# Optimization experiments

Measured on AMD Instinct MI355X. Metric: run time of the kernel, lower is better.

Reference implementation:

```python
import jax, jax.numpy as jnp
import numpy as np

# ---- hyperparameters (from init_kwargs) ----
SIGMA, RHO = 1.0, 10.0
ALPHA, BETA = 1.0, 1.0
K = 3  # ksize; patches are non-overlapping KxK, structure tensor computed on each patch
GRAY_W = np.array([0.2989, 0.587, 0.114], dtype=np.float32)  # torchvision Grayscale weights


def _gauss1d(sigma):
    d = np.arange(-1.0, 2.0, dtype=np.float32)  # radius-1 kernel (fits 3x3 patches)
    g = np.exp(-d * d / (2.0 * sigma * sigma))
    return (g / g.sum()).astype(np.float32)


def _dgauss1d(sigma):
    d = np.arange(-1.0, 2.0, dtype=np.float32)
    g = _gauss1d(sigma)
    return (-d / (sigma * sigma) * g).astype(np.float32)


def _conv3(x, k2d):
    # 'same' zero-padded 3x3 correlation over the last two dims, fully broadcast
    H, W = x.shape[-2], x.shape[-1]
    xp = jnp.pad(x, [(0, 0)] * (x.ndim - 2) + [(1, 1), (1, 1)])
    out = jnp.zeros_like(x)
    for i in range(3):
        for j in range(3):
            out = out + k2d[i, j] * xp[..., i:i + H, j:j + W]
    return out


# precomputed separable kernels (numpy constants)
_G_S, _DG_S, _G_R = _gauss1d(SIGMA), _dgauss1d(SIGMA), _gauss1d(RHO)
_KX = np.outer(_G_S, _DG_S)   # d/dx (last axis), gaussian-smoothed
_KY = np.outer(_DG_S, _G_S)   # d/dy
_KS = np.outer(_G_R, _G_R)    # rho smoothing


def _structure_tensor(gray):
    # gray: (..., K, K) -> (..., 3, K, K) components (Jxx, Jyy, Jxy)
    Ix = _conv3(gray, _KX)
    Iy = _conv3(gray, _KY)
    Jxx = _conv3(Ix * Ix, _KS)
    Jyy = _conv3(Iy * Iy, _KS)
    Jxy = _conv3(Ix * Iy, _KS)
    return jnp.stack([Jxx, Jyy, Jxy], axis=-3)


def _compute_patches(img):
    # img: (B, 3, H, W) -> (B, P, 3*K*K); non-overlapping KxK patches,
    # grayscale -> structure tensor -> per-patch L2 normalize (vectorized, no vmap-of-tiny-ops)
    B, C, H, W = img.shape
    Hb, Wb = H // K, W // K
    p = img.reshape(B, C, Hb, K, Wb, K).transpose(0, 2, 4, 1, 3, 5)  # (B,Hb,Wb,3,K,K)
    p = p.reshape(B, Hb * Wb, C, K, K)
    gray = jnp.einsum('bpchw,c->bphw', p, jnp.asarray(GRAY_W, p.dtype))
    st = _structure_tensor(gray)                                      # (B,P,3,K,K)
    n = jnp.sqrt(jnp.sum(st * st, axis=(-3, -2, -1), keepdims=True)) + 1e-12
    st = st / n
    return st.reshape(B, Hb * Wb, 3 * K * K)


def _resize(img, factor):
    B, C, H, W = img.shape
    return jax.image.resize(img, (B, C, int(H * factor), int(W * factor)),
                            method='bicubic', antialias=False)


def _pairdist_sq(a, b):
    # squared L2 pairwise distance (monotone in L2; only used for argmin)
    aa = jnp.sum(a * a, axis=-1)[:, :, None]
    bb = jnp.sum(b * b, axis=-1)[:, None, :]
    ab = jnp.einsum('bnw,bmw->bnm', a, b)
    return aa + bb - 2.0 * ab


def _loss(x, gt):
    p1 = _compute_patches(x)
    p2 = _compute_patches(gt)
    p2_2 = _compute_patches(_resize(gt, 0.5))
    p2_4 = _compute_patches(_resize(gt, 0.25))
    p2c = jnp.concatenate([p2, p2_2, p2_4], axis=1)      # (B, P2cat, 27)
    score = ALPHA * _pairdist_sq(p1, p2c) + BETA * _pairdist_sq(p2, p2c)
    ind = jnp.argmin(score, axis=2)                      # (B, P1) nearest-neighbor indices
    sel = jnp.take_along_axis(p2c, ind[:, :, None], axis=1)
    return jnp.mean(jnp.abs(p1 - sel))                   # L1 criterion


def setup_inputs() -> dict:
    key = jax.random.key(0)
    k1, k2 = jax.random.split(key)
    x = jax.random.uniform(k1, (4, 3, 192, 192), dtype=jnp.float32)
    gt = jax.random.uniform(k2, (4, 3, 192, 192), dtype=jnp.float32)
    return {'x': x, 'gt': gt}


def reference(x, gt):
    return _loss(x, gt)
```

## Files before the change

kernel.cpp:

```cpp
#include <hip/hip_runtime.h>
#include <hip/hip_bf16.h>
#include <math.h>

namespace {
constexpr int BATCH = 4;
constexpr int IMG   = 192;
constexpr int PL    = IMG * IMG;
constexpr int NP1   = 4096;
constexpr int N96   = 1024;
constexpr int N48   = 256;
constexpr int MALL  = 5376;
constexpr int RS    = 28;
constexpr int NCHUNK = 16;
constexpr int TPC    = 21;

#define GA 0.27406862f
#define GB 0.45186276f
#define RC 0.33277732f
#define RD 0.33444537f

typedef __bf16 bf16x8 __attribute__((ext_vector_type(8)));
typedef float  f32x4  __attribute__((ext_vector_type(4)));

__device__ __forceinline__ void conv3(const float in[9], const float k[9], float out[9]) {
#pragma unroll
  for (int y = 0; y < 3; ++y)
#pragma unroll
    for (int x = 0; x < 3; ++x) {
      float s = 0.f;
#pragma unroll
      for (int i = 0; i < 3; ++i) {
        int yy = y + i - 1;
        if (yy < 0 || yy > 2) continue;
#pragma unroll
        for (int j = 0; j < 3; ++j) {
          int xx = x + j - 1;
          if (xx < 0 || xx > 2) continue;
          s = fmaf(k[i * 3 + j], in[yy * 3 + xx], s);
        }
      }
      out[y * 3 + x] = s;
    }
}

__device__ __forceinline__ void st_from_gray(const float gray[9], float stv[27], float& cs) {
  const float KX[9] = {GA * GA, 0.f, -GA * GA, GB * GA, 0.f, -GB * GA, GA * GA, 0.f, -GA * GA};
  const float KY[9] = {GA * GA, GA * GB, GA * GA, 0.f, 0.f, 0.f, -GA * GA, -GA * GB, -GA * GA};
  const float KS[9] = {RC * RC, RC * RD, RC * RC, RD * RC, RD * RD, RD * RC, RC * RC, RC * RD, RC * RC};
  float Ix[9], Iy[9];
  conv3(gray, KX, Ix);
  conv3(gray, KY, Iy);
  float Pxx[9], Pyy[9], Pxy[9];
#pragma unroll
  for (int t = 0; t < 9; ++t) {
    Pxx[t] = Ix[t] * Ix[t];
    Pyy[t] = Iy[t] * Iy[t];
    Pxy[t] = Ix[t] * Iy[t];
  }
  conv3(Pxx, KS, stv + 0);
  conv3(Pyy, KS, stv + 9);
  conv3(Pxy, KS, stv + 18);
  float s2 = 0.f;
#pragma unroll
  for (int d = 0; d < 27; ++d) s2 = fmaf(stv[d], stv[d], s2);
  float inv = 1.0f / (sqrtf(s2) + 1e-12f);
  float c = 0.f;
#pragma unroll
  for (int d = 0; d < 27; ++d) {
    stv[d] *= inv;
    c = fmaf(stv[d], stv[d], c);
  }
  cs = c;
}

__device__ __forceinline__ void mkw(int k0, int IS, float w[4], int k[4]) {
  const float W4[4] = {-0.0625f, 0.5625f, 0.5625f, -0.0625f};
  float ssum = 0.f;
#pragma unroll
  for (int u = 0; u < 4; ++u) {
    int kk = k0 + u;
    bool v = (kk >= 0) && (kk < IS);
    w[u] = v ? W4[u] : 0.f;
    k[u] = v ? kk : 0;
    ssum += w[u];
  }
  float inv = 1.f / ssum;
#pragma unroll
  for (int u = 0; u < 4; ++u) w[u] *= inv;
}

__device__ __forceinline__ float bicubic_gray(const float* __restrict__ im,
                                              int i, int j, int step, int koff) {
  float wr[4], wc[4];
  int kr[4], kc[4];
  mkw(step * i + koff, IMG, wr, kr);
  mkw(step * j + koff, IMG, wc, kc);
  float acc = 0.f;
#pragma unroll
  for (int u = 0; u < 4; ++u) {
    float rs = 0.f;
#pragma unroll
    for (int v = 0; v < 4; ++v) {
      int o = kr[u] * IMG + kc[v];
      float r  = im[o];
      float g2 = im[PL + o];
      float bl = im[2 * PL + o];
      float gy = fmaf(0.114f, bl, fmaf(0.587f, g2, 0.2989f * r));
      rs = fmaf(wc[v], gy, rs);
    }
    acc = fmaf(wr[u], rs, acc);
  }
  return acc;
}

__device__ __forceinline__ void pack_row(const float v[28], unsigned* __restrict__ dst) {
  unsigned uh[16], ul[16];
#pragma unroll
  for (int p = 0; p < 16; ++p) {
    float a  = (2 * p < 28) ? v[2 * p] : 0.f;
    float bb = (2 * p + 1 < 28) ? v[2 * p + 1] : 0.f;
    __hip_bfloat16 ah = __float2bfloat16(a);
    __hip_bfloat16 bh = __float2bfloat16(bb);
    float af = __bfloat162float(ah), bf2 = __bfloat162float(bh);
    __hip_bfloat16 al = __float2bfloat16(a - af);
    __hip_bfloat16 bl = __float2bfloat16(bb - bf2);
    uh[p] = ((unsigned)__builtin_bit_cast(unsigned short, bh) << 16) |
            (unsigned)__builtin_bit_cast(unsigned short, ah);
    ul[p] = ((unsigned)__builtin_bit_cast(unsigned short, bl) << 16) |
            (unsigned)__builtin_bit_cast(unsigned short, al);
  }
  uint4* d4 = reinterpret_cast<uint4*>(dst);
  d4[0] = make_uint4(uh[0], uh[1], uh[2], uh[3]);
  d4[1] = make_uint4(uh[4], uh[5], uh[6], uh[7]);
  d4[2] = make_uint4(uh[8], uh[9], uh[10], uh[11]);
  d4[3] = make_uint4(uh[12], uh[13], uh[14], uh[15]);
  d4[4] = make_uint4(ul[0], ul[1], ul[2], ul[3]);
  d4[5] = make_uint4(ul[4], ul[5], ul[6], ul[7]);
  d4[6] = make_uint4(ul[8], ul[9], ul[10], ul[11]);
  d4[7] = make_uint4(ul[12], ul[13], ul[14], ul[15]);
}

__device__ __forceinline__ void store_row28(float* __restrict__ dst, const float v[28]) {
  float4* d4 = reinterpret_cast<float4*>(dst);
#pragma unroll
  for (int i = 0; i < 7; ++i)
    d4[i] = make_float4(v[4 * i], v[4 * i + 1], v[4 * i + 2], v[4 * i + 3]);
}

__global__ void __launch_bounds__(256) prep_kernel(
    const float* __restrict__ x, const float* __restrict__ gt,
    float* __restrict__ p1, float* __restrict__ p2c,
    unsigned* __restrict__ Qp, unsigned* __restrict__ Cp,
    unsigned* __restrict__ ctr) {
  int g = blockIdx.x * 256 + threadIdx.x;
  if (g == 0) ctr[0] = 0;

  if (g < BATCH * NP1) {
    int b = g >> 12, p = g & (NP1 - 1);
    int hb = p >> 6, wb = p & 63;
    const size_t boff = (size_t)b * 3 * PL + (size_t)(hb * 3) * IMG + wb * 3;

    float gr[9];
    const float* bx = x + boff;
#pragma unroll
    for (int y = 0; y < 3; ++y)
#pragma unroll
      for (int xx = 0; xx < 3; ++xx) {
        int o = y * IMG + xx;
        gr[y * 3 + xx] = fmaf(0.114f, bx[2 * PL + o], fmaf(0.587f, bx[PL + o], 0.2989f * bx[o]));
      }
    float s1[28];
    float cs1;
    st_from_gray(gr, s1, cs1);
    s1[27] = cs1;

    const float* bg = gt + boff;
#pragma unroll
    for (int y = 0; y < 3; ++y)
#pragma unroll
      for (int xx = 0; xx < 3; ++xx) {
        int o = y * IMG + xx;
        gr[y * 3 + xx] = fmaf(0.114f, bg[2 * PL + o], fmaf(0.587f, bg[PL + o], 0.2989f * bg[o]));
      }
    float s2[28];
    float cs2;
    st_from_gray(gr, s2, cs2);
    s2[27] = cs2;

    store_row28(p1 + (size_t)g * RS, s1);
    size_t crow = (size_t)b * MALL + p;
    store_row28(p2c + crow * RS, s2);

    float vc[28];
#pragma unroll
    for (int d = 0; d < 27; ++d) vc[d] = s2[d];
    vc[27] = -cs2;
    pack_row(vc, Cp + crow * 32);

    float vq[28];
#pragma unroll
    for (int d = 0; d < 27; ++d) vq[d] = s1[d] + s2[d];
    vq[27] = 1.0f;
    pack_row(vq, Qp + (size_t)g * 32);
  } else if (g < BATCH * (NP1 + N96)) {
    int q = g - BATCH * NP1;
    int b = q >> 10, p = q & (N96 - 1);
    int hb = p >> 5, wb = p & 31;
    const float* im = gt + (size_t)b * 3 * PL;
    float gr[9];
#pragma unroll
    for (int y = 0; y < 3; ++y)
#pragma unroll
      for (int xx = 0; xx < 3; ++xx)
        gr[y * 3 + xx] = bicubic_gray(im, 3 * hb + y, 3 * wb + xx, 2, -1);
    float s[28];
    float cs;
    st_from_gray(gr, s, cs);
    s[27] = cs;
    size_t crow = (size_t)b * MALL + NP1 + p;
    store_row28(p2c + crow * RS, s);
    float vc[28];
#pragma unroll
    for (int d = 0; d < 27; ++d) vc[d] = s[d];
    vc[27] = -cs;
    pack_row(vc, Cp + crow * 32);
  } else if (g < BATCH * (NP1 + N96 + N48)) {
    int q = g - BATCH * (NP1 + N96);
    int b = q >> 8, p = q & (N48 - 1);
    int hb = p >> 4, wb = p & 15;
    const float* im = gt + (size_t)b * 3 * PL;
    float gr[9];
#pragma unroll
    for (int y = 0; y < 3; ++y)
#pragma unroll
      for (int xx = 0; xx < 3; ++xx)
        gr[y * 3 + xx] = bicubic_gray(im, 3 * hb + y, 3 * wb + xx, 4, 0);
    float s[28];
    float cs;
    st_from_gray(gr, s, cs);
    s[27] = cs;
    size_t crow = (size_t)b * MALL + NP1 + N96 + p;
    store_row28(p2c + crow * RS, s);
    float vc[28];
#pragma unroll
    for (int d = 0; d < 27; ++d) vc[d] = s[d];
    vc[27] = -cs;
    pack_row(vc, Cp + crow * 32);
  }
}

__global__ void __launch_bounds__(256, 4) argmin_mfma_kernel(
    const unsigned* __restrict__ Qp, const unsigned* __restrict__ Cp,
    float* __restrict__ pscore, int* __restrict__ pidx) {
  const int lane = threadIdx.x & 63;
  const int w = threadIdx.x >> 6;
  const int chunk = blockIdx.y;
  const int b = blockIdx.z;
  const int nbase = blockIdx.x * 256 + w * 64;
  const int lm = lane & 15, lg = lane >> 4;

  bf16x8 qh[4], ql[4];
#pragma unroll
  for (int t = 0; t < 4; ++t) {
    const unsigned* rp = Qp + ((size_t)(b * NP1 + nbase + t * 16 + lm)) * 32 + lg * 4;
    qh[t] = *reinterpret_cast<const bf16x8*>(rp);
    ql[t] = *reinterpret_cast<const bf16x8*>(rp + 16);
  }

  float best[4][4];
  int idx[4][4];
#pragma unroll
  for (int t = 0; t < 4; ++t)
#pragma unroll
    for (int r = 0; r < 4; ++r) { best[t][r] = -INFINITY; idx[t][r] = 0; }

  const int tile0 = chunk * TPC;
  for (int i = 0; i < TPC; ++i) {
    const int m0 = (tile0 + i) * 16;
    const unsigned* cr = Cp + ((size_t)(b * MALL + m0 + lm)) * 32 + lg * 4;
    bf16x8 ch = *reinterpret_cast<const bf16x8*>(cr);
    bf16x8 cl = *reinterpret_cast<const bf16x8*>(cr + 16);
    const int mi = m0 + lm;
#pragma unroll
    for (int t = 0; t < 4; ++t) {
      f32x4 a = {0.f, 0.f, 0.f, 0.f};
      a = __builtin_amdgcn_mfma_f32_16x16x32_bf16(qh[t], ch, a, 0, 0, 0);
      a = __builtin_amdgcn_mfma_f32_16x16x32_bf16(ql[t], ch, a, 0, 0, 0);
      a = __builtin_amdgcn_mfma_f32_16x16x32_bf16(qh[t], cl, a, 0, 0, 0);
#pragma unroll
      for (int r = 0; r < 4; ++r) {
        bool g = a[r] > best[t][r];
        best[t][r] = g ? a[r] : best[t][r];
        idx[t][r] = g ? mi : idx[t][r];
      }
    }
  }

#pragma unroll
  for (int t = 0; t < 4; ++t)
#pragma unroll
    for (int r = 0; r < 4; ++r) {
      float bv = best[t][r];
      int bi = idx[t][r];
#pragma unroll
      for (int mk = 1; mk < 16; mk <<= 1) {
        float ov = __shfl_xor(bv, mk, 64);
        int oi = __shfl_xor(bi, mk, 64);
        bool take = (ov > bv) || (ov == bv && oi < bi);
        bv = take ? ov : bv;
        bi = take ? oi : bi;
      }
      if (lm == 0) {
        int row = nbase + t * 16 + lg * 4 + r;
        size_t o = ((size_t)(b * NP1 + row)) * NCHUNK + chunk;
        pscore[o] = bv;
        pidx[o] = bi;
      }
    }
}

__global__ void __launch_bounds__(256) finalize_kernel(
    const float* __restrict__ p1, const float* __restrict__ p2c,
    const float* __restrict__ pscore, const int* __restrict__ pidx,
    float* __restrict__ bsum, unsigned* __restrict__ ctr, float* __restrict__ out) {
  int g = blockIdx.x * 256 + threadIdx.x;
  float bt = -INFINITY;
  int bi = 0;
  for (int ms = 0; ms < NCHUNK; ++ms) {
    float s = pscore[(size_t)g * NCHUNK + ms];
    int ix = pidx[(size_t)g * NCHUNK + ms];
    bool gg = (s > bt) || (s == bt && ix < bi);
    bt = gg ? s : bt;
    bi = gg ? ix : bi;
  }
  int b = g >> 12;
  const float* a = p1 + (size_t)g * RS;
  const float* s2 = p2c + ((size_t)b * MALL + bi) * RS;
  float acc = 0.f;
#pragma unroll
  for (int d = 0; d < 27; ++d) acc += fabsf(a[d] - s2[d]);

  __shared__ float red[256];
  red[threadIdx.x] = acc;
  __syncthreads();
  for (int st = 128; st > 0; st >>= 1) {
    if (threadIdx.x < st) red[threadIdx.x] += red[threadIdx.x + st];
    __syncthreads();
  }
  if (threadIdx.x == 0) {
    __hip_atomic_store(&bsum[blockIdx.x], red[0], __ATOMIC_RELEASE, __HIP_MEMORY_SCOPE_AGENT);
    unsigned prev = __hip_atomic_fetch_add(ctr, 1u, __ATOMIC_ACQ_REL, __HIP_MEMORY_SCOPE_AGENT);
    if (prev == 63) {
      float s = 0.f;
      for (int i = 0; i < 64; ++i)
        s += __hip_atomic_load(&bsum[i], __ATOMIC_ACQUIRE, __HIP_MEMORY_SCOPE_AGENT);
      out[0] = s * (1.0f / 442368.0f);
    }
  }
}

}

extern "C" void kernel_launch(void* const* d_in, const int* in_sizes, int n_in,
                              void* d_out, int out_size, void* d_ws, size_t ws_size,
                              hipStream_t stream) {
  const float* x  = (const float*)d_in[0];
  const float* gt = (const float*)d_in[1];
  float* out = (float*)d_out;

  float* ws = (float*)d_ws;
  float* p1   = ws;
  float* p2c  = p1 + (size_t)BATCH * NP1 * RS;
  unsigned* Qp = (unsigned*)(p2c + (size_t)BATCH * MALL * RS);
  unsigned* Cp = Qp + (size_t)BATCH * NP1 * 32;
  float* pscore = (float*)(Cp + (size_t)BATCH * MALL * 32);
  int*   pidx   = (int*)(pscore + (size_t)BATCH * NP1 * NCHUNK);
  float* bsum   = (float*)(pidx + (size_t)BATCH * NP1 * NCHUNK);
  unsigned* ctr = (unsigned*)(bsum + 64);

  {
    int tot = BATCH * (NP1 + N96 + N48);
    prep_kernel<<<tot / 256, 256, 0, stream>>>(x, gt, p1, p2c, Qp, Cp, ctr);
  }

  {
    dim3 grid(16, NCHUNK, BATCH);
    argmin_mfma_kernel<<<grid, 256, 0, stream>>>(Qp, Cp, pscore, pidx);
  }

  finalize_kernel<<<(BATCH * NP1) / 256, 256, 0, stream>>>(p1, p2c, pscore, pidx, bsum, ctr, out);
}
```

Before: 74.75 us.

## Restructure prep into LDS-staged and precomputed-resize kernels; pack argmin keys

Splits preprocessing into two kernels. The main one stages three image rows of x and gt in LDS per block and computes the full-resolution patches from there. The same kernel writes bicubic-resized grayscale planes once per pixel, so the scaled patches no longer recompute the 16-tap bicubic per patch pixel. The argmin kernel packs the score and tile index into one unsigned key so each compare is a single max, and moves to 64-thread blocks with a larger grid. Finalize uses 128-thread blocks. This adds a kernel launch and loses 5 mantissa bits when comparing scores, which could change tie-breaking.

```diff
diff --git a/kernel.cpp b/kernel.cpp
--- a/kernel.cpp
+++ b/kernel.cpp
@@ -113,21 +113,26 @@
   return acc;
 }
 
-__device__ __forceinline__ void pack_row(const float v[28], unsigned* __restrict__ dst) {
+__device__ __forceinline__ unsigned bfpair(float a, float b) {
+  __hip_bfloat16 ah = __float2bfloat16(a);
+  __hip_bfloat16 bh = __float2bfloat16(b);
+  return ((unsigned)__builtin_bit_cast(unsigned short, bh) << 16) |
+         (unsigned)__builtin_bit_cast(unsigned short, ah);
+}
+
+__device__ __forceinline__ void pack27(const float* __restrict__ v, float tail,
+                                       unsigned* __restrict__ dst) {
   unsigned uh[16], ul[16];
 #pragma unroll
   for (int p = 0; p < 16; ++p) {
-    float a  = (2 * p < 28) ? v[2 * p] : 0.f;
-    float bb = (2 * p + 1 < 28) ? v[2 * p + 1] : 0.f;
+    float a  = (2 * p < 27) ? v[2 * p] : 0.f;
+    float bb = (2 * p + 1 < 27) ? v[2 * p + 1] : (2 * p + 1 == 27 ? tail : 0.f);
     __hip_bfloat16 ah = __float2bfloat16(a);
     __hip_bfloat16 bh = __float2bfloat16(bb);
     float af = __bfloat162float(ah), bf2 = __bfloat162float(bh);
-    __hip_bfloat16 al = __float2bfloat16(a - af);
-    __hip_bfloat16 bl = __float2bfloat16(bb - bf2);
     uh[p] = ((unsigned)__builtin_bit_cast(unsigned short, bh) << 16) |
             (unsigned)__builtin_bit_cast(unsigned short, ah);
-    ul[p] = ((unsigned)__builtin_bit_cast(unsigned short, bl) << 16) |
-            (unsigned)__builtin_bit_cast(unsigned short, al);
+    ul[p] = bfpair(a - af, bb - bf2);
   }
   uint4* d4 = reinterpret_cast<uint4*>(dst);
   d4[0] = make_uint4(uh[0], uh[1], uh[2], uh[3]);
@@ -140,123 +145,129 @@
   d4[7] = make_uint4(ul[12], ul[13], ul[14], ul[15]);
 }
 
-__device__ __forceinline__ void store_row28(float* __restrict__ dst, const float v[28]) {
+__device__ __forceinline__ void store_row28(float* __restrict__ dst, const float v[27], float tail) {
   float4* d4 = reinterpret_cast<float4*>(dst);
 #pragma unroll
-  for (int i = 0; i < 7; ++i)
+  for (int i = 0; i < 6; ++i)
     d4[i] = make_float4(v[4 * i], v[4 * i + 1], v[4 * i + 2], v[4 * i + 3]);
-}
-
-__global__ void __launch_bounds__(256) prep_kernel(
+  d4[6] = make_float4(v[24], v[25], v[26], tail);
+}
+
+__global__ void __launch_bounds__(64) prep_main_kernel(
     const float* __restrict__ x, const float* __restrict__ gt,
     float* __restrict__ p1, float* __restrict__ p2c,
     unsigned* __restrict__ Qp, unsigned* __restrict__ Cp,
+    float* __restrict__ g96, float* __restrict__ g48,
     unsigned* __restrict__ ctr) {
-  int g = blockIdx.x * 256 + threadIdx.x;
-  if (g == 0) ctr[0] = 0;
-
-  if (g < BATCH * NP1) {
-    int b = g >> 12, p = g & (NP1 - 1);
-    int hb = p >> 6, wb = p & 63;
-    const size_t boff = (size_t)b * 3 * PL + (size_t)(hb * 3) * IMG + wb * 3;
-
-    float gr[9];
-    const float* bx = x + boff;
-#pragma unroll
-    for (int y = 0; y < 3; ++y)
-#pragma unroll
-      for (int xx = 0; xx < 3; ++xx) {
-        int o = y * IMG + xx;
-        gr[y * 3 + xx] = fmaf(0.114f, bx[2 * PL + o], fmaf(0.587f, bx[PL + o], 0.2989f * bx[o]));
-      }
-    float s1[28];
-    float cs1;
-    st_from_gray(gr, s1, cs1);
-    s1[27] = cs1;
-
-    const float* bg = gt + boff;
-#pragma unroll
-    for (int y = 0; y < 3; ++y)
-#pragma unroll
-      for (int xx = 0; xx < 3; ++xx) {
-        int o = y * IMG + xx;
-        gr[y * 3 + xx] = fmaf(0.114f, bg[2 * PL + o], fmaf(0.587f, bg[PL + o], 0.2989f * bg[o]));
-      }
-    float s2[28];
-    float cs2;
-    st_from_gray(gr, s2, cs2);
-    s2[27] = cs2;
-
-    store_row28(p1 + (size_t)g * RS, s1);
-    size_t crow = (size_t)b * MALL + p;
-    store_row28(p2c + crow * RS, s2);
-
-    float vc[28];
-#pragma unroll
-    for (int d = 0; d < 27; ++d) vc[d] = s2[d];
-    vc[27] = -cs2;
-    pack_row(vc, Cp + crow * 32);
-
-    float vq[28];
-#pragma unroll
-    for (int d = 0; d < 27; ++d) vq[d] = s1[d] + s2[d];
-    vq[27] = 1.0f;
-    pack_row(vq, Qp + (size_t)g * 32);
-  } else if (g < BATCH * (NP1 + N96)) {
-    int q = g - BATCH * NP1;
+  const int bid = blockIdx.x;
+  const int t = threadIdx.x;
+  if (bid == 0 && t == 0) ctr[0] = 0;
+
+  if (bid < 256) {
+    const int b = bid >> 6, hb = bid & 63;
+    __shared__ float lds[3456];
+    for (int it = 0; it < 54; ++it) {
+      int idx = it * 64 + t;
+      int img = idx / 1728;
+      int rem = idx - img * 1728;
+      int c = rem / 576; rem -= c * 576;
+      int r = rem / 192; int col = rem - r * 192;
+      const float* sp = (img == 0) ? x : gt;
+      lds[idx] = sp[(size_t)b * 3 * PL + (size_t)c * PL + (size_t)(hb * 3 + r) * IMG + col];
+    }
+    __syncthreads();
+
+    float s1[27], s2[27];
+    float cs1, cs2;
+    {
+      float gr[9];
+#pragma unroll
+      for (int y = 0; y < 3; ++y)
+#pragma unroll
+        for (int xx = 0; xx < 3; ++xx) {
+          int o = y * 192 + 3 * t + xx;
+          gr[y * 3 + xx] = fmaf(0.114f, lds[1152 + o], fmaf(0.587f, lds[576 + o], 0.2989f * lds[o]));
+        }
+      st_from_gray(gr, s1, cs1);
+    }
+    {
+      float gr[9];
+#pragma unroll
+      for (int y = 0; y < 3; ++y)
+#pragma unroll
+        for (int xx = 0; xx < 3; ++xx) {
+          int o = 1728 + y * 192 + 3 * t + xx;
+          gr[y * 3 + xx] = fmaf(0.114f, lds[1152 + o], fmaf(0.587f, lds[576 + o], 0.2989f * lds[o]));
+        }
+      st_from_gray(gr, s2, cs2);
+    }
+
+    const int p = hb * 64 + t;
+    const int g = b * NP1 + p;
+    const size_t crow = (size_t)b * MALL + p;
+    store_row28(p1 + (size_t)g * RS, s1, cs1);
+    store_row28(p2c + crow * RS, s2, cs2);
+    pack27(s2, -cs2, Cp + crow * 32);
+    float qs[27];
+#pragma unroll
+    for (int d = 0; d < 27; ++d) qs[d] = s1[d] + s2[d];
+    pack27(qs, 1.0f, Qp + (size_t)g * 32);
+  } else {
+    int pix = (bid - 256) * 64 + t;
+    if (pix < BATCH * 9216) {
+      int b = pix / 9216, rem = pix - b * 9216;
+      int i = rem / 96, j = rem - i * 96;
+      g96[pix] = bicubic_gray(gt + (size_t)b * 3 * PL, i, j, 2, -1);
+    } else {
+      int q = pix - BATCH * 9216;
+      int b = q / 2304, rem = q - b * 2304;
+      int i = rem / 48, j = rem - i * 48;
+      g48[q] = bicubic_gray(gt + (size_t)b * 3 * PL, i, j, 4, 0);
+    }
+  }
+}
+
+__global__ void __launch_bounds__(64) prep_scaled_kernel(
+    const float* __restrict__ g96, const float* __restrict__ g48,
+    float* __restrict__ p2c, unsigned* __restrict__ Cp) {
+  int q = blockIdx.x * 64 + threadIdx.x;
+  const float* gp;
+  int S, row;
+  int hb, wb;
+  if (q < BATCH * N96) {
     int b = q >> 10, p = q & (N96 - 1);
-    int hb = p >> 5, wb = p & 31;
-    const float* im = gt + (size_t)b * 3 * PL;
-    float gr[9];
-#pragma unroll
-    for (int y = 0; y < 3; ++y)
-#pragma unroll
-      for (int xx = 0; xx < 3; ++xx)
-        gr[y * 3 + xx] = bicubic_gray(im, 3 * hb + y, 3 * wb + xx, 2, -1);
-    float s[28];
-    float cs;
-    st_from_gray(gr, s, cs);
-    s[27] = cs;
-    size_t crow = (size_t)b * MALL + NP1 + p;
-    store_row28(p2c + crow * RS, s);
-    float vc[28];
-#pragma unroll
-    for (int d = 0; d < 27; ++d) vc[d] = s[d];
-    vc[27] = -cs;
-    pack_row(vc, Cp + crow * 32);
-  } else if (g < BATCH * (NP1 + N96 + N48)) {
-    int q = g - BATCH * (NP1 + N96);
-    int b = q >> 8, p = q & (N48 - 1);
-    int hb = p >> 4, wb = p & 15;
-    const float* im = gt + (size_t)b * 3 * PL;
-    float gr[9];
-#pragma unroll
-    for (int y = 0; y < 3; ++y)
-#pragma unroll
-      for (int xx = 0; xx < 3; ++xx)
-        gr[y * 3 + xx] = bicubic_gray(im, 3 * hb + y, 3 * wb + xx, 4, 0);
-    float s[28];
-    float cs;
-    st_from_gray(gr, s, cs);
-    s[27] = cs;
-    size_t crow = (size_t)b * MALL + NP1 + N96 + p;
-    store_row28(p2c + crow * RS, s);
-    float vc[28];
-#pragma unroll
-    for (int d = 0; d < 27; ++d) vc[d] = s[d];
-    vc[27] = -cs;
-    pack_row(vc, Cp + crow * 32);
-  }
-}
-
-__global__ void __launch_bounds__(256, 4) argmin_mfma_kernel(
+    hb = p >> 5; wb = p & 31;
+    gp = g96 + (size_t)b * 9216;
+    S = 96;
+    row = b * MALL + NP1 + p;
+  } else {
+    int q2 = q - BATCH * N96;
+    int b = q2 >> 8, p = q2 & (N48 - 1);
+    hb = p >> 4; wb = p & 15;
+    gp = g48 + (size_t)b * 2304;
+    S = 48;
+    row = b * MALL + NP1 + N96 + p;
+  }
+  float gr[9];
+#pragma unroll
+  for (int y = 0; y < 3; ++y)
+#pragma unroll
+    for (int xx = 0; xx < 3; ++xx)
+      gr[y * 3 + xx] = gp[(size_t)(3 * hb + y) * S + 3 * wb + xx];
+  float s[27];
+  float cs;
+  st_from_gray(gr, s, cs);
+  store_row28(p2c + (size_t)row * RS, s, cs);
+  pack27(s, -cs, Cp + (size_t)row * 32);
+}
+
+__global__ void __launch_bounds__(64, 4) argmin_mfma_kernel(
     const unsigned* __restrict__ Qp, const unsigned* __restrict__ Cp,
-    float* __restrict__ pscore, int* __restrict__ pidx) {
-  const int lane = threadIdx.x & 63;
-  const int w = threadIdx.x >> 6;
+    unsigned* __restrict__ pkey, int* __restrict__ pidx) {
+  const int lane = threadIdx.x;
   const int chunk = blockIdx.y;
   const int b = blockIdx.z;
-  const int nbase = blockIdx.x * 256 + w * 64;
+  const int nbase = blockIdx.x * 64;
   const int lm = lane & 15, lg = lane >> 4;
 
   bf16x8 qh[4], ql[4];
@@ -267,31 +278,30 @@
     ql[t] = *reinterpret_cast<const bf16x8*>(rp + 16);
   }
 
-  float best[4][4];
-  int idx[4][4];
+  unsigned keys[4][4];
 #pragma unroll
   for (int t = 0; t < 4; ++t)
 #pragma unroll
-    for (int r = 0; r < 4; ++r) { best[t][r] = -INFINITY; idx[t][r] = 0; }
+    for (int r = 0; r < 4; ++r) keys[t][r] = 0u;
 
   const int tile0 = chunk * TPC;
+  const unsigned* cr = Cp + ((size_t)(b * MALL + tile0 * 16 + lm)) * 32 + lg * 4;
+#pragma unroll 3
   for (int i = 0; i < TPC; ++i) {
-    const int m0 = (tile0 + i) * 16;
-    const unsigned* cr = Cp + ((size_t)(b * MALL + m0 + lm)) * 32 + lg * 4;
     bf16x8 ch = *reinterpret_cast<const bf16x8*>(cr);
     bf16x8 cl = *reinterpret_cast<const bf16x8*>(cr + 16);
-    const int mi = m0 + lm;
+    cr += 16 * 32;
 #pragma unroll
     for (int t = 0; t < 4; ++t) {
-      f32x4 a = {0.f, 0.f, 0.f, 0.f};
+      f32x4 a = {4.f, 4.f, 4.f, 4.f};
       a = __builtin_amdgcn_mfma_f32_16x16x32_bf16(qh[t], ch, a, 0, 0, 0);
       a = __builtin_amdgcn_mfma_f32_16x16x32_bf16(ql[t], ch, a, 0, 0, 0);
       a = __builtin_amdgcn_mfma_f32_16x16x32_bf16(qh[t], cl, a, 0, 0, 0);
 #pragma unroll
       for (int r = 0; r < 4; ++r) {
-        bool g = a[r] > best[t][r];
-        best[t][r] = g ? a[r] : best[t][r];
-        idx[t][r] = g ? mi : idx[t][r];
+        unsigned kb = (__builtin_bit_cast(unsigned, (float)a[r]) & 0xFFFFFFE0u) |
+                      (31u - (unsigned)i);
+        keys[t][r] = keys[t][r] > kb ? keys[t][r] : kb;
       }
     }
   }
@@ -300,37 +310,37 @@
   for (int t = 0; t < 4; ++t)
 #pragma unroll
     for (int r = 0; r < 4; ++r) {
-      float bv = best[t][r];
-      int bi = idx[t][r];
+      unsigned k = keys[t][r];
+      int m = (tile0 + (int)(31u - (k & 31u))) * 16 + lm;
 #pragma unroll
       for (int mk = 1; mk < 16; mk <<= 1) {
-        float ov = __shfl_xor(bv, mk, 64);
-        int oi = __shfl_xor(bi, mk, 64);
-        bool take = (ov > bv) || (ov == bv && oi < bi);
-        bv = take ? ov : bv;
-        bi = take ? oi : bi;
+        unsigned ok = (unsigned)__shfl_xor((int)k, mk, 64);
+        int om = __shfl_xor(m, mk, 64);
+        bool take = (ok > k) || (ok == k && om < m);
+        k = take ? ok : k;
+        m = take ? om : m;
       }
       if (lm == 0) {
-        int row = nbase + t * 16 + lg * 4 + r;
-        size_t o = ((size_t)(b * NP1 + row)) * NCHUNK + chunk;
-        pscore[o] = bv;
-        pidx[o] = bi;
+        int rowi = nbase + t * 16 + lg * 4 + r;
+        size_t o = ((size_t)(b * NP1 + rowi)) * NCHUNK + chunk;
+        pkey[o] = k & 0xFFFFFFE0u;
+        pidx[o] = m;
       }
     }
 }
 
-__global__ void __launch_bounds__(256) finalize_kernel(
+__global__ void __launch_bounds__(128) finalize_kernel(
     const float* __restrict__ p1, const float* __restrict__ p2c,
-    const float* __restrict__ pscore, const int* __restrict__ pidx,
+    const unsigned* __restrict__ pkey, const int* __restrict__ pidx,
     float* __restrict__ bsum, unsigned* __restrict__ ctr, float* __restrict__ out) {
-  int g = blockIdx.x * 256 + threadIdx.x;
-  float bt = -INFINITY;
+  int g = blockIdx.x * 128 + threadIdx.x;
+  unsigned bk = 0u;
   int bi = 0;
   for (int ms = 0; ms < NCHUNK; ++ms) {
-    float s = pscore[(size_t)g * NCHUNK + ms];
+    unsigned k = pkey[(size_t)g * NCHUNK + ms];
     int ix = pidx[(size_t)g * NCHUNK + ms];
-    bool gg = (s > bt) || (s == bt && ix < bi);
-    bt = gg ? s : bt;
+    bool gg = k > bk;
+    bk = gg ? k : bk;
     bi = gg ? ix : bi;
   }
   int b = g >> 12;
@@ -340,19 +350,19 @@
 #pragma unroll
   for (int d = 0; d < 27; ++d) acc += fabsf(a[d] - s2[d]);
 
-  __shared__ float red[256];
+  __shared__ float red[128];
   red[threadIdx.x] = acc;
   __syncthreads();
-  for (int st = 128; st > 0; st >>= 1) {
+  for (int st = 64; st > 0; st >>= 1) {
     if (threadIdx.x < st) red[threadIdx.x] += red[threadIdx.x + st];
     __syncthreads();
   }
   if (threadIdx.x == 0) {
     __hip_atomic_store(&bsum[blockIdx.x], red[0], __ATOMIC_RELEASE, __HIP_MEMORY_SCOPE_AGENT);
     unsigned prev = __hip_atomic_fetch_add(ctr, 1u, __ATOMIC_ACQ_REL, __HIP_MEMORY_SCOPE_AGENT);
-    if (prev == 63) {
+    if (prev == 127) {
       float s = 0.f;
-      for (int i = 0; i < 64; ++i)
+      for (int i = 0; i < 128; ++i)
         s += __hip_atomic_load(&bsum[i], __ATOMIC_ACQUIRE, __HIP_MEMORY_SCOPE_AGENT);
       out[0] = s * (1.0f / 442368.0f);
     }
@@ -373,20 +383,21 @@
   float* p2c  = p1 + (size_t)BATCH * NP1 * RS;
   unsigned* Qp = (unsigned*)(p2c + (size_t)BATCH * MALL * RS);
   unsigned* Cp = Qp + (size_t)BATCH * NP1 * 32;
-  float* pscore = (float*)(Cp + (size_t)BATCH * MALL * 32);
-  int*   pidx   = (int*)(pscore + (size_t)BATCH * NP1 * NCHUNK);
+  float* g96  = (float*)(Cp + (size_t)BATCH * MALL * 32);
+  float* g48  = g96 + (size_t)BATCH * 9216;
+  unsigned* pkey = (unsigned*)(g48 + (size_t)BATCH * 2304);
+  int*   pidx   = (int*)(pkey + (size_t)BATCH * NP1 * NCHUNK);
   float* bsum   = (float*)(pidx + (size_t)BATCH * NP1 * NCHUNK);
-  unsigned* ctr = (unsigned*)(bsum + 64);
+  unsigned* ctr = (unsigned*)(bsum + 128);
+
+  prep_main_kernel<<<976, 64, 0, stream>>>(x, gt, p1, p2c, Qp, Cp, g96, g48, ctr);
+
+  prep_scaled_kernel<<<80, 64, 0, stream>>>(g96, g48, p2c, Cp);
 
   {
-    int tot = BATCH * (NP1 + N96 + N48);
-    prep_kernel<<<tot / 256, 256, 0, stream>>>(x, gt, p1, p2c, Qp, Cp, ctr);
-  }
-
-  {
-    dim3 grid(16, NCHUNK, BATCH);
-    argmin_mfma_kernel<<<grid, 256, 0, stream>>>(Qp, Cp, pscore, pidx);
-  }
-
-  finalize_kernel<<<(BATCH * NP1) / 256, 256, 0, stream>>>(p1, p2c, pscore, pidx, bsum, ctr, out);
-}
+    dim3 grid(64, NCHUNK, BATCH);
+    argmin_mfma_kernel<<<grid, 64, 0, stream>>>(Qp, Cp, pkey, pidx);
+  }
+
+  finalize_kernel<<<128, 128, 0, stream>>>(p1, p2c, pkey, pidx, bsum, ctr, out);
+}
```

Result: slower. 86.91 us (+16.3%).
